# Kernel tuning notes

Measured on AMD Instinct MI355X. Metric: run time of the kernel, lower is better.

Reference implementation:

```python
import jax, jax.numpy as jnp
import numpy as np

NUM_HEADS = 8
WEIGHTS_DIM = 512
INPUT_DIM = 512
D_HEAD = WEIGHTS_DIM // NUM_HEADS


def setup_inputs() -> dict:
    key = jax.random.key(0)
    ks = jax.random.split(key, 9)
    B, S, D = 4, 2048, INPUT_DIM
    s_in = 1.0 / np.sqrt(D)
    s_w = 1.0 / np.sqrt(WEIGHTS_DIM)
    return {
        "x": jax.random.normal(ks[0], (B, S, D), dtype=jnp.float32),
        "Wq": jax.random.normal(ks[1], (D, WEIGHTS_DIM), dtype=jnp.float32) * s_in,
        "bq": jnp.zeros((WEIGHTS_DIM,), dtype=jnp.float32),
        "Wk": jax.random.normal(ks[2], (D, WEIGHTS_DIM), dtype=jnp.float32) * s_in,
        "bk": jnp.zeros((WEIGHTS_DIM,), dtype=jnp.float32),
        "Wv": jax.random.normal(ks[3], (D, WEIGHTS_DIM), dtype=jnp.float32) * s_in,
        "bv": jnp.zeros((WEIGHTS_DIM,), dtype=jnp.float32),
        "Wh": jax.random.normal(ks[4], (WEIGHTS_DIM, D), dtype=jnp.float32) * s_w,
        "bh": jnp.zeros((D,), dtype=jnp.float32),
    }


def _split_heads(t):
    # [B, S, Dm] -> [B, H, S, d_head]
    B, S, _ = t.shape
    return t.reshape(B, S, NUM_HEADS, D_HEAD).transpose(0, 2, 1, 3)


def reference(x, Wq, bq, Wk, bk, Wv, bv, Wh, bh):
    q = _split_heads(x @ Wq + bq)
    k = _split_heads(x @ Wk + bk)
    v = _split_heads(x @ Wv + bv)
    scale = 1.0 / jnp.sqrt(jnp.float32(D_HEAD))
    scores = jnp.einsum("bhqd,bhkd->bhqk", q, k) * scale  # [B,H,S,S]
    weights = jax.nn.softmax(scores, axis=-1)
    attn = jnp.einsum("bhqk,bhkd->bhqd", weights, v)
    B, H, S, d = attn.shape
    concat = attn.transpose(0, 2, 1, 3).reshape(B, S, H * d)
    return concat @ Wh + bh
```

## Files before the change

kernel.cpp:

```cpp
#include <hip/hip_runtime.h>
#include <stdint.h>

#define NB  4
#define SS  2048
#define DD  512
#define HH  8
#define DHH 64
#define MM  (NB * SS)

typedef __attribute__((ext_vector_type(8))) short bf16x8;
typedef __attribute__((ext_vector_type(4))) float f32x4;
typedef __attribute__((ext_vector_type(4))) short s16x4;

union fu32 { float f; unsigned u; };
union pfu  { uint4 u; bf16x8 v; };

static __device__ __forceinline__ short f2bf(float f) {
  fu32 a; a.f = f;
  unsigned u = a.u;
  return (short)((u + 0x7fffu + ((u >> 16) & 1u)) >> 16);
}
static __device__ __forceinline__ float bf2f(short s) {
  fu32 t; t.u = ((unsigned)(unsigned short)s) << 16;
  return t.f;
}

static __device__ __forceinline__ void async16(const void* g, void* l) {
  __builtin_amdgcn_global_load_lds(
      (__attribute__((address_space(1))) unsigned*)(void*)g,
      (__attribute__((address_space(3))) unsigned*)l, 16, 0, 0);
}

__global__ __launch_bounds__(256) void prep_kernel(
    const float* __restrict__ x, short* __restrict__ xb,
    const float* __restrict__ W0, const float* __restrict__ W1,
    const float* __restrict__ W2, const float* __restrict__ W3,
    short* __restrict__ T0, short* __restrict__ T1,
    short* __restrict__ T2, short* __restrict__ T3) {
  const int bid = blockIdx.x, tid = threadIdx.x;
  if (bid < 2048) {
    int i = (bid * 256 + tid) * 8;
    float4 v0 = *(const float4*)(x + i);
    float4 v1 = *(const float4*)(x + i + 4);
    bf16x8 o;
    o[0] = f2bf(v0.x); o[1] = f2bf(v0.y); o[2] = f2bf(v0.z); o[3] = f2bf(v0.w);
    o[4] = f2bf(v1.x); o[5] = f2bf(v1.y); o[6] = f2bf(v1.z); o[7] = f2bf(v1.w);
    *(bf16x8*)(xb + i) = o;
  } else {
    int z = bid - 2048;
    int widx = z >> 6, rem = z & 63;
    const float* W = widx == 0 ? W0 : widx == 1 ? W1 : widx == 2 ? W2 : W3;
    short*       T = widx == 0 ? T0 : widx == 1 ? T1 : widx == 2 ? T2 : T3;
    int n  = (rem & 7) * 64 + (tid & 63);
    int k0 = (rem >> 3) * 64 + (tid >> 6) * 16;
    bf16x8 t0, t1;
#pragma unroll
    for (int j = 0; j < 8; ++j) t0[j] = f2bf(W[(size_t)(k0 + j) * DD + n]);
#pragma unroll
    for (int j = 0; j < 8; ++j) t1[j] = f2bf(W[(size_t)(k0 + 8 + j) * DD + n]);
    *(bf16x8*)(T + (size_t)n * DD + k0)     = t0;
    *(bf16x8*)(T + (size_t)n * DD + k0 + 8) = t1;
  }
}

__global__ __launch_bounds__(256, 4) void gemm_qkv_kernel(
    const short* __restrict__ A, const short* __restrict__ Bt,
    const float* __restrict__ bq, const float* __restrict__ bk,
    const float* __restrict__ bv, short* __restrict__ qout,
    short* __restrict__ kout, short* __restrict__ vtout, float qscale) {
  __shared__ __align__(16) short a_sh[64 * 64];
  __shared__ __align__(16) short b_sh[128 * 64];
  const int tid  = threadIdx.x;
  const int w    = tid >> 6, lane = tid & 63, quad = lane >> 4, l16 = lane & 15;
  const int m0   = blockIdx.y * 64, n0 = blockIdx.x * 128;
  const int mw   = (w >> 1) * 32,   nw = (w & 1) * 64;
  const int rw   = lane >> 3, seg = lane & 7, gs = seg ^ rw;
  const int sxz  = l16 & 7;

  f32x4 acc[2][4];
#pragma unroll
  for (int i = 0; i < 2; ++i)
#pragma unroll
    for (int j = 0; j < 4; ++j) acc[i][j] = {0.f, 0.f, 0.f, 0.f};

  for (int kt = 0; kt < DD; kt += 64) {
    __syncthreads();
    {
      const short* ga = A  + (size_t)(m0 + w * 16 + rw) * DD + kt + gs * 8;
      const short* gb = Bt + (size_t)(n0 + w * 32 + rw) * DD + kt + gs * 8;
#pragma unroll
      for (int i = 0; i < 2; ++i)
        async16(ga + (size_t)i * 8 * DD, &a_sh[(w * 16 + i * 8) * 64]);
#pragma unroll
      for (int i = 0; i < 4; ++i)
        async16(gb + (size_t)i * 8 * DD, &b_sh[(w * 32 + i * 8) * 64]);
    }
    __syncthreads();
#pragma unroll
    for (int ks = 0; ks < 2; ++ks) {
      const int so = ((ks * 4 + quad) ^ sxz) * 8;
      bf16x8 af[2], bfr[4];
#pragma unroll
      for (int mt = 0; mt < 2; ++mt)
        af[mt] = *(const bf16x8*)&a_sh[(mw + mt * 16 + l16) * 64 + so];
#pragma unroll
      for (int nt = 0; nt < 4; ++nt)
        bfr[nt] = *(const bf16x8*)&b_sh[(nw + nt * 16 + l16) * 64 + so];
#pragma unroll
      for (int mt = 0; mt < 2; ++mt)
#pragma unroll
        for (int nt = 0; nt < 4; ++nt)
          acc[mt][nt] = __builtin_amdgcn_mfma_f32_16x16x32_bf16(
              af[mt], bfr[nt], acc[mt][nt], 0, 0, 0);
    }
  }

#pragma unroll
  for (int nt = 0; nt < 4; ++nt) {
    const int n   = n0 + nw + nt * 16 + l16;
    const int sg  = n >> 9, n9 = n & 511, h = n9 >> 6, d = n & 63;
    const float bval = (sg == 0 ? bq : sg == 1 ? bk : bv)[n9];
    const float scl  = (sg == 0) ? qscale : 1.0f;
#pragma unroll
    for (int mt = 0; mt < 2; ++mt) {
      const int mb = m0 + mw + mt * 16 + quad * 4;
      const int bi = mb >> 11, s = mb & (SS - 1);
      if (sg == 2) {
        s16x4 pk;
#pragma unroll
        for (int r = 0; r < 4; ++r) pk[r] = f2bf(acc[mt][nt][r] + bval);
        *(s16x4*)&vtout[((size_t)(bi * HH + h) * DHH + d) * SS + s] = pk;
      } else {
        short* o = (sg == 0) ? qout : kout;
        const size_t base = ((size_t)(bi * HH + h) * SS + s) * DHH + d;
#pragma unroll
        for (int r = 0; r < 4; ++r)
          o[base + (size_t)r * DHH] = f2bf((acc[mt][nt][r] + bval) * scl);
      }
    }
  }
}

__global__ __launch_bounds__(256, 2) void attn_kernel(
    const short* __restrict__ Qa, const short* __restrict__ Ka,
    const short* __restrict__ Vt, short* __restrict__ Op0,
    short* __restrict__ Op1, float* __restrict__ lpw) {
  __shared__ __align__(16) short k_sh[128 * 64];
  __shared__ __align__(16) short vt_sh[64 * 128];

  const int tid  = threadIdx.x;
  const int w    = tid >> 6, lane = tid & 63, quad = lane >> 4, l16 = lane & 15;
  const int n    = blockIdx.x;
  const int grp  = (n & 7) * 8 + ((n >> 3) & 7);
  const int qt_b = n >> 6;
  const int half = grp & 1, h = (grp >> 1) & 7, b = grp >> 4;
  const int q0   = qt_b * 256;
  const int rw = lane >> 3, seg = lane & 7, gs = seg ^ rw;
  const int sxz = l16 & 7;
  const size_t base = (size_t)(b * HH + h) * SS * DHH;
  const short* Qg = Qa + base + (size_t)(q0 + w * 64) * DHH;
  const short* Kg = Ka + base;
  const short* Vg = Vt + base;

  bf16x8 qf[4][2];
#pragma unroll
  for (int qt = 0; qt < 4; ++qt)
#pragma unroll
    for (int ks = 0; ks < 2; ++ks)
      qf[qt][ks] = *(const bf16x8*)(Qg + (size_t)(qt * 16 + l16) * DHH + ks * 32 + quad * 8);

  bf16x8 ones;
#pragma unroll
  for (int j = 0; j < 8; ++j) ones[j] = (short)0x3F80;

  f32x4 o_acc[4][4];
#pragma unroll
  for (int qt = 0; qt < 4; ++qt)
#pragma unroll
    for (int dt = 0; dt < 4; ++dt) o_acc[qt][dt] = {0.f, 0.f, 0.f, 0.f};
  f32x4 l_acc[4];
#pragma unroll
  for (int qt = 0; qt < 4; ++qt) l_acc[qt] = {0.f, 0.f, 0.f, 0.f};

  const int addrA = ((((quad & 1) << 1) + (quad >> 1)) * 16 + l16) * 4;
  const int addrB = addrA ^ 64;
  const bool qeven = (quad & 1) == 0;

  const int kstart = half * (SS / 2);

  for (int kb = kstart; kb < kstart + SS / 2; kb += 128) {
    __syncthreads();
    {
      const short* gk = Kg + (size_t)(kb + w * 32 + rw) * DHH + gs * 8;
#pragma unroll
      for (int i = 0; i < 4; ++i)
        async16(gk + (size_t)i * 8 * DHH, &k_sh[(w * 32 + i * 8) * 64]);
#pragma unroll
      for (int i = 0; i < 4; ++i) {
        const int d = w * 16 + i * 4 + (lane >> 4);
        const int gseg = (lane & 15) ^ (d & 15);
        async16(Vg + (size_t)d * SS + kb + gseg * 8,
                &vt_sh[(w * 16 + i * 4) * 128]);
      }
    }
    __syncthreads();

#pragma unroll
    for (int ck = 0; ck < 4; ++ck) {
      uint2 pk[4][2];
#pragma unroll
      for (int t = 0; t < 2; ++t) {
        const int knt = ck * 2 + t;
        bf16x8 kf0 = *(const bf16x8*)&k_sh[(knt * 16 + l16) * 64 + ((0 * 4 + quad) ^ sxz) * 8];
        bf16x8 kf1 = *(const bf16x8*)&k_sh[(knt * 16 + l16) * 64 + ((1 * 4 + quad) ^ sxz) * 8];
#pragma unroll
        for (int qt = 0; qt < 4; ++qt) {
          f32x4 s = {0.f, 0.f, 0.f, 0.f};
          s = __builtin_amdgcn_mfma_f32_16x16x32_bf16(kf0, qf[qt][0], s, 0, 0, 0);
          s = __builtin_amdgcn_mfma_f32_16x16x32_bf16(kf1, qf[qt][1], s, 0, 0, 0);
          fu32 e0, e1, e2, e3;
          e0.f = __builtin_amdgcn_exp2f(s[0]);
          e1.f = __builtin_amdgcn_exp2f(s[1]);
          e2.f = __builtin_amdgcn_exp2f(s[2]);
          e3.f = __builtin_amdgcn_exp2f(s[3]);
          pk[qt][t].x = __builtin_amdgcn_perm(e1.u, e0.u, 0x07060302u);
          pk[qt][t].y = __builtin_amdgcn_perm(e3.u, e2.u, 0x07060302u);
        }
      }
      bf16x8 vf[4];
#pragma unroll
      for (int dt = 0; dt < 4; ++dt)
        vf[dt] = *(const bf16x8*)&vt_sh[(dt * 16 + l16) * 128 + ((ck * 4 + quad) ^ l16) * 8];
#pragma unroll
      for (int qt = 0; qt < 4; ++qt) {
        unsigned p1x = (unsigned)__shfl_xor((int)pk[qt][1].x, 16);
        unsigned p1y = (unsigned)__shfl_xor((int)pk[qt][1].y, 16);
        unsigned v0x = qeven ? pk[qt][0].x : p1x;
        unsigned v0y = qeven ? pk[qt][0].y : p1y;
        unsigned v2x = qeven ? p1x : pk[qt][0].x;
        unsigned v2y = qeven ? p1y : pk[qt][0].y;
        pfu pf;
        pf.u.x = (unsigned)__builtin_amdgcn_ds_bpermute(addrA, (int)v0x);
        pf.u.y = (unsigned)__builtin_amdgcn_ds_bpermute(addrA, (int)v0y);
        pf.u.z = (unsigned)__builtin_amdgcn_ds_bpermute(addrB, (int)v2x);
        pf.u.w = (unsigned)__builtin_amdgcn_ds_bpermute(addrB, (int)v2y);
        l_acc[qt] = __builtin_amdgcn_mfma_f32_16x16x32_bf16(pf.v, ones, l_acc[qt], 0, 0, 0);
#pragma unroll
        for (int dt = 0; dt < 4; ++dt)
          o_acc[qt][dt] = __builtin_amdgcn_mfma_f32_16x16x32_bf16(pf.v, vf[dt], o_acc[qt][dt], 0, 0, 0);
      }
    }
  }

  short* Op = half ? Op1 : Op0;
#pragma unroll
  for (int qt = 0; qt < 4; ++qt) {
#pragma unroll
    for (int r = 0; r < 4; ++r) {
      const int qg = q0 + w * 64 + qt * 16 + quad * 4 + r;
      const size_t row = (size_t)(b * HH + h) * SS + qg;
      if (l16 == 0)
        lpw[(size_t)half * (NB * HH * SS) + row] = l_acc[qt][r];
      const float inv = __builtin_amdgcn_rcpf(l_acc[qt][r]);
#pragma unroll
      for (int dt = 0; dt < 4; ++dt)
        Op[row * DHH + dt * 16 + l16] = f2bf(o_acc[qt][dt][r] * inv);
    }
  }
}

__global__ __launch_bounds__(256, 4) void gemm_proj_kernel(
    const short* __restrict__ Op0, const short* __restrict__ Op1,
    const float* __restrict__ lpw, const short* __restrict__ Bt,
    const float* __restrict__ bias, float* __restrict__ out) {
  __shared__ __align__(16) short a0_sh[64 * 64];
  __shared__ __align__(16) short a1_sh[64 * 64];
  __shared__ __align__(16) short b_sh[64 * 64];
  const int tid = threadIdx.x;
  const int w   = tid >> 6, lane = tid & 63, quad = lane >> 4, l16 = lane & 15;
  const int m0  = blockIdx.y * 64, n0 = blockIdx.x * 64;
  const int mw  = (w >> 1) * 32, nw = (w & 1) * 32;
  const int rw  = lane >> 3, seg = lane & 7, gs = seg ^ rw;
  const int sxz = l16 & 7;
  const int bb  = m0 >> 11, q0 = m0 & (SS - 1);

  f32x4 acc[2][2];
#pragma unroll
  for (int i = 0; i < 2; ++i)
#pragma unroll
    for (int j = 0; j < 2; ++j) acc[i][j] = {0.f, 0.f, 0.f, 0.f};

  for (int kt = 0; kt < DD; kt += 64) {
    const int h = kt >> 6;
    const size_t lbase = (size_t)(bb * HH + h) * SS + q0;
    const size_t abase = lbase * DHH;
    __syncthreads();
    {
      const short* g0 = Op0 + abase + (size_t)(w * 16 + rw) * DHH + gs * 8;
      const short* g1 = Op1 + abase + (size_t)(w * 16 + rw) * DHH + gs * 8;
      const short* gb = Bt + (size_t)(n0 + w * 16 + rw) * DD + kt + gs * 8;
#pragma unroll
      for (int i = 0; i < 2; ++i) {
        async16(g0 + (size_t)i * 8 * DHH, &a0_sh[(w * 16 + i * 8) * 64]);
        async16(g1 + (size_t)i * 8 * DHH, &a1_sh[(w * 16 + i * 8) * 64]);
        async16(gb + (size_t)i * 8 * DD,  &b_sh[(w * 16 + i * 8) * 64]);
      }
    }
    float w1[2], w2[2];
#pragma unroll
    for (int mt = 0; mt < 2; ++mt) {
      const size_t lrow = lbase + mw + mt * 16 + l16;
      const float l1 = lpw[lrow];
      const float l2 = lpw[(size_t)NB * HH * SS + lrow];
      const float inv = __builtin_amdgcn_rcpf(l1 + l2);
      w1[mt] = l1 * inv; w2[mt] = l2 * inv;
    }
    __syncthreads();
#pragma unroll
    for (int ks = 0; ks < 2; ++ks) {
      const int so = ((ks * 4 + quad) ^ sxz) * 8;
      pfu af[2];
#pragma unroll
      for (int mt = 0; mt < 2; ++mt) {
        bf16x8 a0 = *(const bf16x8*)&a0_sh[(mw + mt * 16 + l16) * 64 + so];
        bf16x8 a1 = *(const bf16x8*)&a1_sh[(mw + mt * 16 + l16) * 64 + so];
        unsigned* rp = (unsigned*)&af[mt];
#pragma unroll
        for (int jp = 0; jp < 4; ++jp) {
          fu32 f0, f1;
          f0.f = w1[mt] * bf2f(a0[2 * jp])     + w2[mt] * bf2f(a1[2 * jp]);
          f1.f = w1[mt] * bf2f(a0[2 * jp + 1]) + w2[mt] * bf2f(a1[2 * jp + 1]);
          rp[jp] = __builtin_amdgcn_perm(f1.u, f0.u, 0x07060302u);
        }
      }
#pragma unroll
      for (int nt = 0; nt < 2; ++nt) {
        bf16x8 bfr = *(const bf16x8*)&b_sh[(nw + nt * 16 + l16) * 64 + so];
        acc[0][nt] = __builtin_amdgcn_mfma_f32_16x16x32_bf16(af[0].v, bfr, acc[0][nt], 0, 0, 0);
        acc[1][nt] = __builtin_amdgcn_mfma_f32_16x16x32_bf16(af[1].v, bfr, acc[1][nt], 0, 0, 0);
      }
    }
  }

#pragma unroll
  for (int nt = 0; nt < 2; ++nt) {
    const int   n  = n0 + nw + nt * 16 + l16;
    const float bv = bias[n];
#pragma unroll
    for (int mt = 0; mt < 2; ++mt)
#pragma unroll
      for (int r = 0; r < 4; ++r) {
        const int m = m0 + mw + mt * 16 + quad * 4 + r;
        out[(size_t)m * DD + n] = acc[mt][nt][r] + bv;
      }
  }
}

extern "C" void kernel_launch(void* const* d_in, const int* in_sizes, int n_in,
                              void* d_out, int out_size, void* d_ws, size_t ws_size,
                              hipStream_t stream) {
  (void)in_sizes; (void)n_in; (void)out_size; (void)ws_size;
  const float* x  = (const float*)d_in[0];
  const float* Wq = (const float*)d_in[1];
  const float* bq = (const float*)d_in[2];
  const float* Wk = (const float*)d_in[3];
  const float* bk = (const float*)d_in[4];
  const float* Wv = (const float*)d_in[5];
  const float* bv = (const float*)d_in[6];
  const float* Wh = (const float*)d_in[7];
  const float* bh = (const float*)d_in[8];

  short* ws  = (short*)d_ws;
  short* xb  = ws;
  short* wqt = xb  + (size_t)MM * DD;
  short* wkt = wqt + (size_t)DD * DD;
  short* wvt = wkt + (size_t)DD * DD;
  short* wht = wvt + (size_t)DD * DD;
  short* qws = wht + (size_t)DD * DD;
  short* kws = qws + (size_t)MM * DD;
  short* vws = kws + (size_t)MM * DD;
  short* op1 = vws + (size_t)MM * DD;
  float* lpw = (float*)(op1 + (size_t)MM * DD);

  hipLaunchKernelGGL(prep_kernel, dim3(2048 + 256), dim3(256), 0, stream,
                     x, xb, Wq, Wk, Wv, Wh, wqt, wkt, wvt, wht);

  const float qscale = 1.4426950408889634f / 8.0f;
  hipLaunchKernelGGL(gemm_qkv_kernel, dim3(12, 128), dim3(256), 0, stream,
                     xb, wqt, bq, bk, bv, qws, kws, vws, qscale);

  hipLaunchKernelGGL(attn_kernel, dim3(512), dim3(256), 0, stream,
                     qws, kws, vws, xb, op1, lpw);

  hipLaunchKernelGGL(gemm_proj_kernel, dim3(8, 128), dim3(256), 0, stream,
                     xb, op1, lpw, wht, bh, (float*)d_out);
}
```

Measured before the change: 177.1 us.

## Stage QKV epilogue through LDS for coalesced stores; double attention KV tile

The QKV GEMM epilogue now writes the biased, scaled bf16 results into shared memory (padded rows), then emits coalesced 16-byte stores for Q/K and for the transposed V, instead of scattered 2-byte and 8-byte stores. The attention kernel's K/V tile grows from 128 to 256 keys per iteration with a wider XOR swizzle, halving the number of barrier/load phases. This raises LDS usage in the attention kernel to 64KB per block, which may reduce occupancy, and adds extra barriers to the GEMM epilogue.

```diff
diff --git a/kernel.cpp b/kernel.cpp
--- a/kernel.cpp
+++ b/kernel.cpp
@@ -68,8 +68,9 @@
     const float* __restrict__ bq, const float* __restrict__ bk,
     const float* __restrict__ bv, short* __restrict__ qout,
     short* __restrict__ kout, short* __restrict__ vtout, float qscale) {
-  __shared__ __align__(16) short a_sh[64 * 64];
-  __shared__ __align__(16) short b_sh[128 * 64];
+  __shared__ __align__(16) short sh[64 * 64 + 128 * 64];
+  short* a_sh = sh;
+  short* b_sh = sh + 64 * 64;
   const int tid  = threadIdx.x;
   const int w    = tid >> 6, lane = tid & 63, quad = lane >> 4, l16 = lane & 15;
   const int m0   = blockIdx.y * 64, n0 = blockIdx.x * 128;
@@ -115,28 +116,53 @@
     }
   }
 
-#pragma unroll
-  for (int nt = 0; nt < 4; ++nt) {
-    const int n   = n0 + nw + nt * 16 + l16;
-    const int sg  = n >> 9, n9 = n & 511, h = n9 >> 6, d = n & 63;
-    const float bval = (sg == 0 ? bq : sg == 1 ? bk : bv)[n9];
-    const float scl  = (sg == 0) ? qscale : 1.0f;
-#pragma unroll
-    for (int mt = 0; mt < 2; ++mt) {
-      const int mb = m0 + mw + mt * 16 + quad * 4;
-      const int bi = mb >> 11, s = mb & (SS - 1);
-      if (sg == 2) {
-        s16x4 pk;
-#pragma unroll
-        for (int r = 0; r < 4; ++r) pk[r] = f2bf(acc[mt][nt][r] + bval);
-        *(s16x4*)&vtout[((size_t)(bi * HH + h) * DHH + d) * SS + s] = pk;
-      } else {
-        short* o = (sg == 0) ? qout : kout;
-        const size_t base = ((size_t)(bi * HH + h) * SS + s) * DHH + d;
+  __syncthreads();
+  const int sgb = n0 >> 9;
+  const int h0  = (n0 & 511) >> 6;
+  const int bi  = m0 >> 11, s0 = m0 & (SS - 1);
+  if (sgb < 2) {
+    const float* bias = (sgb == 0) ? bq : bk;
+    const float  scl  = (sgb == 0) ? qscale : 1.0f;
+#pragma unroll
+    for (int nt = 0; nt < 4; ++nt) {
+      const int dl = nw + nt * 16 + l16;
+      const float bval = bias[(n0 & 511) + dl];
+#pragma unroll
+      for (int mt = 0; mt < 2; ++mt)
 #pragma unroll
         for (int r = 0; r < 4; ++r)
-          o[base + (size_t)r * DHH] = f2bf((acc[mt][nt][r] + bval) * scl);
-      }
+          sh[(mw + mt * 16 + quad * 4 + r) * 136 + dl] =
+              f2bf((acc[mt][nt][r] + bval) * scl);
+    }
+    __syncthreads();
+    short* o = (sgb == 0) ? qout : kout;
+#pragma unroll
+    for (int i = 0; i < 4; ++i) {
+      const int c = tid + 256 * i;
+      const int s = c >> 4, d8 = (c & 15) * 8;
+      const int hh = h0 + (d8 >> 6), dd = d8 & 63;
+      *(bf16x8*)&o[((size_t)(bi * HH + hh) * SS + s0 + s) * DHH + dd] =
+          *(const bf16x8*)&sh[s * 136 + d8];
+    }
+  } else {
+#pragma unroll
+    for (int nt = 0; nt < 4; ++nt) {
+      const int dl = nw + nt * 16 + l16;
+      const float bval = bv[(n0 & 511) + dl];
+#pragma unroll
+      for (int mt = 0; mt < 2; ++mt)
+#pragma unroll
+        for (int r = 0; r < 4; ++r)
+          sh[dl * 72 + mw + mt * 16 + quad * 4 + r] = f2bf(acc[mt][nt][r] + bval);
+    }
+    __syncthreads();
+#pragma unroll
+    for (int i = 0; i < 4; ++i) {
+      const int c = tid + 256 * i;
+      const int d = c >> 3, s8 = (c & 7) * 8;
+      const int hh = h0 + (d >> 6), dd = d & 63;
+      *(bf16x8*)&vtout[((size_t)(bi * HH + hh) * DHH + dd) * SS + s0 + s8] =
+          *(const bf16x8*)&sh[d * 72 + s8];
     }
   }
 }
@@ -145,8 +171,8 @@
     const short* __restrict__ Qa, const short* __restrict__ Ka,
     const short* __restrict__ Vt, short* __restrict__ Op0,
     short* __restrict__ Op1, float* __restrict__ lpw) {
-  __shared__ __align__(16) short k_sh[128 * 64];
-  __shared__ __align__(16) short vt_sh[64 * 128];
+  __shared__ __align__(16) short k_sh[256 * 64];
+  __shared__ __align__(16) short vt_sh[64 * 256];
 
   const int tid  = threadIdx.x;
   const int w    = tid >> 6, lane = tid & 63, quad = lane >> 4, l16 = lane & 15;
@@ -188,25 +214,25 @@
 
   const int kstart = half * (SS / 2);
 
-  for (int kb = kstart; kb < kstart + SS / 2; kb += 128) {
+  for (int kb = kstart; kb < kstart + SS / 2; kb += 256) {
     __syncthreads();
     {
-      const short* gk = Kg + (size_t)(kb + w * 32 + rw) * DHH + gs * 8;
-#pragma unroll
-      for (int i = 0; i < 4; ++i)
-        async16(gk + (size_t)i * 8 * DHH, &k_sh[(w * 32 + i * 8) * 64]);
-#pragma unroll
-      for (int i = 0; i < 4; ++i) {
-        const int d = w * 16 + i * 4 + (lane >> 4);
-        const int gseg = (lane & 15) ^ (d & 15);
-        async16(Vg + (size_t)d * SS + kb + gseg * 8,
-                &vt_sh[(w * 16 + i * 4) * 128]);
-      }
-    }
-    __syncthreads();
-
-#pragma unroll
-    for (int ck = 0; ck < 4; ++ck) {
+      const short* gk = Kg + (size_t)(kb + w * 64 + rw) * DHH + gs * 8;
+#pragma unroll
+      for (int i = 0; i < 8; ++i)
+        async16(gk + (size_t)i * 8 * DHH, &k_sh[(w * 64 + i * 8) * 64]);
+#pragma unroll
+      for (int i = 0; i < 8; ++i) {
+        const int d = w * 16 + i * 2 + (lane >> 5);
+        const int kseg = (lane & 31) ^ (d & 31);
+        async16(Vg + (size_t)d * SS + kb + kseg * 8,
+                &vt_sh[(w * 16 + i * 2) * 256]);
+      }
+    }
+    __syncthreads();
+
+#pragma unroll
+    for (int ck = 0; ck < 8; ++ck) {
       uint2 pk[4][2];
 #pragma unroll
       for (int t = 0; t < 2; ++t) {
@@ -229,8 +255,10 @@
       }
       bf16x8 vf[4];
 #pragma unroll
-      for (int dt = 0; dt < 4; ++dt)
-        vf[dt] = *(const bf16x8*)&vt_sh[(dt * 16 + l16) * 128 + ((ck * 4 + quad) ^ l16) * 8];
+      for (int dt = 0; dt < 4; ++dt) {
+        const int dl = dt * 16 + l16;
+        vf[dt] = *(const bf16x8*)&vt_sh[dl * 256 + ((ck * 4 + quad) ^ (dl & 31)) * 8];
+      }
 #pragma unroll
       for (int qt = 0; qt < 4; ++qt) {
         unsigned p1x = (unsigned)__shfl_xor((int)pk[qt][1].x, 16);
```

New measurement: 171.8 us. 3.0% less time.
